# Kernel tuning notes

Hardware: AMD Instinct MI355X
Metric: run time of the kernel (lower is better)

Reference implementation:

```python
import jax, jax.numpy as jnp
import numpy as np


def setup_inputs() -> dict:
    key = jax.random.key(0)
    k1, k2, k3 = jax.random.split(key, 3)
    B, C, H, W = 4, 32, 320, 320
    NC = 21  # num_category
    return {
        "input_F": jax.random.normal(k1, (B, C, H, W), dtype=jnp.float32),
        "input_logit": jax.random.normal(k2, (B, NC, H, W), dtype=jnp.float32),
        "weight": jnp.asarray(1.0, dtype=jnp.float32),
        "compatibility": jax.random.normal(k3, (NC, NC, 1, 1), dtype=jnp.float32) * 0.1,
        "bias": jnp.zeros((NC,), dtype=jnp.float32),
        "kernel_len": 7,
    }


def _local_crf_pass(input_F, Q, weight, kernel_len):
    # Fused local_diff + exp-kernel + local_crf aggregation.
    # For each of the k*k neighborhood offsets (zero padding):
    #   diff[b,h,w]  = sum_c (F[b,c,h,w] - F_shift[b,c,h,w])^2 / C
    #   kern[b,h,w]  = weight * exp(-diff)
    #   out[b,q,h,w] += kern * Q_shift[b,q,h,w]
    B, C, H, W = input_F.shape
    pad = kernel_len // 2
    Fp = jnp.pad(input_F, ((0, 0), (0, 0), (pad, pad), (pad, pad)))
    Qp = jnp.pad(Q, ((0, 0), (0, 0), (pad, pad), (pad, pad)))
    out = jnp.zeros_like(Q)
    inv_c = jnp.float32(1.0 / C)
    for di in range(kernel_len):
        for dj in range(kernel_len):
            Fs = Fp[:, :, di:di + H, dj:dj + W]
            diff = jnp.sum((input_F - Fs) ** 2, axis=1) * inv_c  # [B,H,W]
            kern = weight * jnp.exp(-diff)
            out = out + kern[:, None, :, :] * Qp[:, :, di:di + H, dj:dj + W]
    return out / jnp.float32(kernel_len)


def reference(input_F, input_logit, weight, compatibility, bias, kernel_len):
    Q = jax.nn.softmax(input_logit, axis=1)  # softmax over categories
    out = _local_crf_pass(input_F, Q, weight, kernel_len)  # [B,NC,H,W]
    # 1x1 conv with sigmoid(compatibility) + bias
    compat = jax.nn.sigmoid(compatibility[:, :, 0, 0])  # [NC_out, NC_in]
    out = jnp.einsum('oi,bihw->bohw', compat, out) + bias[None, :, None, None]
    return input_logit - out
```

## Files before the change

### kernel.cpp

```cpp
#include <hip/hip_runtime.h>

#define Bn 4
#define Cn 32
#define Hn 320
#define Wn 320
#define NCn 21
#define PADn 3
#define TH 16
#define TW 64
#define HH 22
#define HWID 70
#define FW 71
#define QSTR 76
#define C2n 16
#define HWSZ (Hn*Wn)

typedef _Float16 h2 __attribute__((ext_vector_type(2)));

#define F_WORDS (C2n*HH*FW)
#define LDS_Q_OFF (F_WORDS*4)
#define LDS_TOTAL (LDS_Q_OFF + NCn*HH*QSTR)

__global__ __launch_bounds__(256, 1) void crf_fused(
    const float* __restrict__ Fin, const float* __restrict__ logit,
    const float* __restrict__ weight, const float* __restrict__ compat,
    const float* __restrict__ bias, float* __restrict__ out)
{
  extern __shared__ char smem[];
  uint32_t* fbuf = (uint32_t*)smem;
  uint8_t*  qbuf = (uint8_t*)(smem + LDS_Q_OFF);

  const int bid = blockIdx.x;
  const int b   = bid / 100;
  const int r   = bid % 100;
  const int th  = r / 5, twi = r % 5;
  const int h0  = th * TH, w0 = twi * TW;
  const int tid = threadIdx.x;

  const float* fb0 = Fin + (size_t)b * Cn * HWSZ;
  for (int idx = tid; idx < C2n * HH * HWID; idx += 256) {
    int lw = idx % HWID;
    int t2 = idx / HWID;
    int lh = t2 % HH;
    int c2 = t2 / HH;
    int gh = h0 - PADn + lh, gw = w0 - PADn + lw;
    uint32_t wd = 0u;
    if ((unsigned)gh < (unsigned)Hn && (unsigned)gw < (unsigned)Wn) {
      const float* p = fb0 + (size_t)(2 * c2) * HWSZ + gh * Wn + gw;
      float a0 = p[0], a1 = p[HWSZ];
      h2 hp; hp[0] = (_Float16)a0; hp[1] = (_Float16)a1;
      wd = __builtin_bit_cast(uint32_t, hp);
    }
    fbuf[(c2 * HH + lh) * FW + lw] = wd;
  }

  const float* lg0 = logit + (size_t)b * NCn * HWSZ;
  for (int p = tid; p < HH * HWID; p += 256) {
    int lw = p % HWID, lh = p / HWID;
    int gh = h0 - PADn + lh, gw = w0 - PADn + lw;
    uint8_t* qp = qbuf + lh * QSTR + lw;
    if ((unsigned)gh < (unsigned)Hn && (unsigned)gw < (unsigned)Wn) {
      const float* lp = lg0 + gh * Wn + gw;
      float v[NCn];
      float m = -1e30f;
      #pragma unroll
      for (int o = 0; o < NCn; o++) { v[o] = lp[(size_t)o * HWSZ]; m = fmaxf(m, v[o]); }
      float s = 0.f;
      #pragma unroll
      for (int o = 0; o < NCn; o++) { v[o] = __expf(v[o] - m); s += v[o]; }
      float inv = 1.0f / s;
      #pragma unroll
      for (int o = 0; o < NCn; o++) {
        int pk = __builtin_amdgcn_cvt_pk_fp8_f32(v[o] * inv, 0.f, 0, false);
        qp[o * HH * QSTR] = (uint8_t)(pk & 0xff);
      }
    } else {
      #pragma unroll
      for (int o = 0; o < NCn; o++) qp[o * HH * QSTR] = 0;
    }
  }
  __syncthreads();

  const int ty = tid >> 4;
  const int tg = tid & 15;
  const int x  = tg << 2;

  float acc[4][NCn];
  #pragma unroll
  for (int p = 0; p < 4; p++)
    #pragma unroll
    for (int o = 0; o < NCn; o++) acc[p][o] = 0.f;

  #pragma unroll 1
  for (int di = 0; di < 7; di++) {
    const int lhn = ty + di;
    float dsum[4][7];
    #pragma unroll
    for (int p = 0; p < 4; p++)
      #pragma unroll
      for (int j = 0; j < 7; j++) dsum[p][j] = 0.f;

    #pragma unroll 2
    for (int c2 = 0; c2 < C2n; c2++) {
      const uint32_t* frow = fbuf + (c2 * HH + lhn) * FW + x;
      const uint32_t* fcen = fbuf + (c2 * HH + (ty + PADn)) * FW + x + PADn;
      uint32_t nw[10], cw[4];
      #pragma unroll
      for (int j = 0; j < 10; j++) nw[j] = frow[j];
      #pragma unroll
      for (int p = 0; p < 4; p++) cw[p] = fcen[p];
      #pragma unroll
      for (int p = 0; p < 4; p++) {
        h2 c = __builtin_bit_cast(h2, cw[p]);
        #pragma unroll
        for (int j = 0; j < 7; j++) {
          h2 n = __builtin_bit_cast(h2, nw[p + j]);
          h2 d = c - n;
#if __has_builtin(__builtin_amdgcn_fdot2)
          dsum[p][j] = __builtin_amdgcn_fdot2(d, d, dsum[p][j], false);
#else
          float d0 = (float)d[0], d1 = (float)d[1];
          dsum[p][j] += d0 * d0 + d1 * d1;
#endif
        }
      }
    }
    #pragma unroll
    for (int p = 0; p < 4; p++)
      #pragma unroll
      for (int j = 0; j < 7; j++)
        dsum[p][j] = __expf(dsum[p][j] * -0.03125f);

    #pragma unroll
    for (int o = 0; o < NCn; o++) {
      const uint32_t* qrow = (const uint32_t*)(qbuf + (o * HH + lhn) * QSTR + x);
      uint32_t q0 = qrow[0], q1 = qrow[1], q2 = qrow[2];
      float qv[10];
      qv[0] = __builtin_amdgcn_cvt_f32_fp8((int)q0, 0);
      qv[1] = __builtin_amdgcn_cvt_f32_fp8((int)q0, 1);
      qv[2] = __builtin_amdgcn_cvt_f32_fp8((int)q0, 2);
      qv[3] = __builtin_amdgcn_cvt_f32_fp8((int)q0, 3);
      qv[4] = __builtin_amdgcn_cvt_f32_fp8((int)q1, 0);
      qv[5] = __builtin_amdgcn_cvt_f32_fp8((int)q1, 1);
      qv[6] = __builtin_amdgcn_cvt_f32_fp8((int)q1, 2);
      qv[7] = __builtin_amdgcn_cvt_f32_fp8((int)q1, 3);
      qv[8] = __builtin_amdgcn_cvt_f32_fp8((int)q2, 0);
      qv[9] = __builtin_amdgcn_cvt_f32_fp8((int)q2, 1);
      #pragma unroll
      for (int p = 0; p < 4; p++)
        #pragma unroll
        for (int j = 0; j < 7; j++)
          acc[p][o] = fmaf(dsum[p][j], qv[p + j], acc[p][o]);
    }
  }

  __syncthreads();
  float* cmat = (float*)(smem + LDS_Q_OFF);
  {
    float wgt = weight[0] * (1.0f / 7.0f);
    for (int i = tid; i < NCn * NCn; i += 256) {
      float c = compat[i];
      cmat[i] = wgt / (1.f + __expf(-c));
    }
  }
  __syncthreads();

  const int gh = h0 + ty;
  const size_t pixoff = (size_t)b * NCn * HWSZ + (size_t)gh * Wn + (w0 + x);
  const float* lc = logit + pixoff;
  float* oc = out + pixoff;
  #pragma unroll
  for (int o = 0; o < NCn; o++) {
    float s0 = 0.f, s1 = 0.f, s2 = 0.f, s3 = 0.f;
    #pragma unroll
    for (int i2 = 0; i2 < NCn; i2++) {
      float cm = cmat[o * NCn + i2];
      s0 = fmaf(cm, acc[0][i2], s0);
      s1 = fmaf(cm, acc[1][i2], s1);
      s2 = fmaf(cm, acc[2][i2], s2);
      s3 = fmaf(cm, acc[3][i2], s3);
    }
    float bo = bias[o];
    const float4 lg = *(const float4*)(lc + (size_t)o * HWSZ);
    float4 rr;
    rr.x = lg.x - s0 - bo;
    rr.y = lg.y - s1 - bo;
    rr.z = lg.z - s2 - bo;
    rr.w = lg.w - s3 - bo;
    *(float4*)(oc + (size_t)o * HWSZ) = rr;
  }
}

extern "C" void kernel_launch(void* const* d_in, const int* in_sizes, int n_in,
                              void* d_out, int out_size, void* d_ws, size_t ws_size,
                              hipStream_t stream) {
  (void)in_sizes; (void)n_in; (void)out_size; (void)d_ws; (void)ws_size;
  const float* F      = (const float*)d_in[0];
  const float* logit  = (const float*)d_in[1];
  const float* weight = (const float*)d_in[2];
  const float* compat = (const float*)d_in[3];
  const float* bias   = (const float*)d_in[4];
  float* out = (float*)d_out;

  hipFuncSetAttribute((const void*)crf_fused,
                      hipFuncAttributeMaxDynamicSharedMemorySize, LDS_TOTAL);
  crf_fused<<<dim3(Bn * 100), dim3(256), LDS_TOTAL, stream>>>(
      F, logit, weight, compat, bias, out);
}
```

Before: 283.8 us.

## Store features as FP8 in LDS, enlarge tile to 32x64, cache center features

After: 250.7 us. 11.7% less time.

```diff
diff --git a/kernel.cpp b/kernel.cpp
--- a/kernel.cpp
+++ b/kernel.cpp
@@ -5,60 +5,80 @@
 #define Hn 320
 #define Wn 320
 #define NCn 21
-#define PADn 3
-#define TH 16
-#define TW 64
-#define HH 22
-#define HWID 70
-#define FW 71
-#define QSTR 76
-#define C2n 16
 #define HWSZ (Hn*Wn)
 
+#define THr 32
+#define TWr 64
+#define HHr 38
+#define HWIDr 70
+#define FWr 72
+#define NG 8
+#define QSTRr 76
+
 typedef _Float16 h2 __attribute__((ext_vector_type(2)));
 
-#define F_WORDS (C2n*HH*FW)
-#define LDS_Q_OFF (F_WORDS*4)
-#define LDS_TOTAL (LDS_Q_OFF + NCn*HH*QSTR)
-
-__global__ __launch_bounds__(256, 1) void crf_fused(
+#define LDS_F   (NG*HHr*FWr*4)
+#define LDS_Q   (NCn*HHr*QSTRr)
+#define LDS_TOTAL (LDS_F + LDS_Q)
+
+__device__ __forceinline__ h2 fp8pair_lo(uint32_t w) {
+  uint32_t t = ((w & 0x000000FFu) << 8) | ((w & 0x0000FF00u) << 16);
+  uint32_t r = (t & 0x80008000u) | ((t >> 1) & 0x3FFF3FFFu);
+  return __builtin_bit_cast(h2, r);
+}
+__device__ __forceinline__ h2 fp8pair_hi(uint32_t w) {
+  uint32_t t = ((w >> 8) & 0x0000FF00u) | (w & 0xFF000000u);
+  uint32_t r = (t & 0x80008000u) | ((t >> 1) & 0x3FFF3FFFu);
+  return __builtin_bit_cast(h2, r);
+}
+
+__device__ __forceinline__ float fdot2f(h2 a, h2 b, float c) {
+#if __has_builtin(__builtin_amdgcn_fdot2)
+  return __builtin_amdgcn_fdot2(a, b, c, false);
+#else
+  return c + (float)a[0]*(float)b[0] + (float)a[1]*(float)b[1];
+#endif
+}
+
+__global__ __launch_bounds__(512, 1) void crf_fused2(
     const float* __restrict__ Fin, const float* __restrict__ logit,
     const float* __restrict__ weight, const float* __restrict__ compat,
     const float* __restrict__ bias, float* __restrict__ out)
 {
   extern __shared__ char smem[];
   uint32_t* fbuf = (uint32_t*)smem;
-  uint8_t*  qbuf = (uint8_t*)(smem + LDS_Q_OFF);
+  uint8_t*  qbuf = (uint8_t*)(smem + LDS_F);
 
   const int bid = blockIdx.x;
-  const int b   = bid / 100;
-  const int r   = bid % 100;
+  const int b   = bid / 50;
+  const int r   = bid % 50;
   const int th  = r / 5, twi = r % 5;
-  const int h0  = th * TH, w0 = twi * TW;
+  const int h0  = th * THr, w0 = twi * TWr;
   const int tid = threadIdx.x;
 
   const float* fb0 = Fin + (size_t)b * Cn * HWSZ;
-  for (int idx = tid; idx < C2n * HH * HWID; idx += 256) {
-    int lw = idx % HWID;
-    int t2 = idx / HWID;
-    int lh = t2 % HH;
-    int c2 = t2 / HH;
-    int gh = h0 - PADn + lh, gw = w0 - PADn + lw;
+  for (int idx = tid; idx < NG * HHr * FWr; idx += 512) {
+    int lw = idx % FWr;
+    int r2 = idx / FWr;
+    int lh = r2 % HHr;
+    int g  = r2 / HHr;
+    int gh = h0 - 3 + lh, gw = w0 - 3 + lw;
     uint32_t wd = 0u;
-    if ((unsigned)gh < (unsigned)Hn && (unsigned)gw < (unsigned)Wn) {
-      const float* p = fb0 + (size_t)(2 * c2) * HWSZ + gh * Wn + gw;
-      float a0 = p[0], a1 = p[HWSZ];
-      h2 hp; hp[0] = (_Float16)a0; hp[1] = (_Float16)a1;
-      wd = __builtin_bit_cast(uint32_t, hp);
-    }
-    fbuf[(c2 * HH + lh) * FW + lw] = wd;
+    if (lw < HWIDr && (unsigned)gh < (unsigned)Hn && (unsigned)gw < (unsigned)Wn) {
+      const float* p = fb0 + (size_t)(4 * g) * HWSZ + gh * Wn + gw;
+      float f0 = p[0], f1 = p[HWSZ], f2 = p[2 * HWSZ], f3 = p[3 * HWSZ];
+      int pk = __builtin_amdgcn_cvt_pk_fp8_f32(f0, f1, 0, false);
+      pk = __builtin_amdgcn_cvt_pk_fp8_f32(f2, f3, pk, true);
+      wd = (uint32_t)pk;
+    }
+    fbuf[idx] = wd;
   }
 
   const float* lg0 = logit + (size_t)b * NCn * HWSZ;
-  for (int p = tid; p < HH * HWID; p += 256) {
-    int lw = p % HWID, lh = p / HWID;
-    int gh = h0 - PADn + lh, gw = w0 - PADn + lw;
-    uint8_t* qp = qbuf + lh * QSTR + lw;
+  for (int p = tid; p < HHr * HWIDr; p += 512) {
+    int lw = p % HWIDr, lh = p / HWIDr;
+    int gh = h0 - 3 + lh, gw = w0 - 3 + lw;
+    uint8_t* qp = qbuf + lh * QSTRr + lw;
     if ((unsigned)gh < (unsigned)Hn && (unsigned)gw < (unsigned)Wn) {
       const float* lp = lg0 + gh * Wn + gw;
       float v[NCn];
@@ -72,11 +92,11 @@
       #pragma unroll
       for (int o = 0; o < NCn; o++) {
         int pk = __builtin_amdgcn_cvt_pk_fp8_f32(v[o] * inv, 0.f, 0, false);
-        qp[o * HH * QSTR] = (uint8_t)(pk & 0xff);
+        qp[(size_t)o * HHr * QSTRr] = (uint8_t)(pk & 0xff);
       }
     } else {
       #pragma unroll
-      for (int o = 0; o < NCn; o++) qp[o * HH * QSTR] = 0;
+      for (int o = 0; o < NCn; o++) qp[(size_t)o * HHr * QSTRr] = 0;
     }
   }
   __syncthreads();
@@ -85,6 +105,18 @@
   const int tg = tid & 15;
   const int x  = tg << 2;
 
+  h2 cen[NG][8];
+  #pragma unroll
+  for (int g = 0; g < NG; g++) {
+    const uint32_t* fc = fbuf + (g * HHr + (ty + 3)) * FWr + (x + 3);
+    #pragma unroll
+    for (int p = 0; p < 4; p++) {
+      uint32_t w = fc[p];
+      cen[g][2 * p]     = fp8pair_lo(w);
+      cen[g][2 * p + 1] = fp8pair_hi(w);
+    }
+  }
+
   float acc[4][NCn];
   #pragma unroll
   for (int p = 0; p < 4; p++)
@@ -94,46 +126,46 @@
   #pragma unroll 1
   for (int di = 0; di < 7; di++) {
     const int lhn = ty + di;
-    float dsum[4][7];
+    float ds[4][7];
     #pragma unroll
     for (int p = 0; p < 4; p++)
       #pragma unroll
-      for (int j = 0; j < 7; j++) dsum[p][j] = 0.f;
-
-    #pragma unroll 2
-    for (int c2 = 0; c2 < C2n; c2++) {
-      const uint32_t* frow = fbuf + (c2 * HH + lhn) * FW + x;
-      const uint32_t* fcen = fbuf + (c2 * HH + (ty + PADn)) * FW + x + PADn;
-      uint32_t nw[10], cw[4];
-      #pragma unroll
-      for (int j = 0; j < 10; j++) nw[j] = frow[j];
-      #pragma unroll
-      for (int p = 0; p < 4; p++) cw[p] = fcen[p];
-      #pragma unroll
-      for (int p = 0; p < 4; p++) {
-        h2 c = __builtin_bit_cast(h2, cw[p]);
+      for (int j = 0; j < 7; j++) ds[p][j] = 0.f;
+
+    #pragma unroll
+    for (int g = 0; g < NG; g++) {
+      const uint32_t* frow = fbuf + (g * HHr + lhn) * FWr + x;
+      uint4 n0 = *(const uint4*)(frow);
+      uint4 n1 = *(const uint4*)(frow + 4);
+      uint4 n2 = *(const uint4*)(frow + 8);
+      uint32_t nw[10] = {n0.x, n0.y, n0.z, n0.w, n1.x, n1.y, n1.z, n1.w, n2.x, n2.y};
+      #pragma unroll
+      for (int k = 0; k < 10; k++) {
+        h2 lo = fp8pair_lo(nw[k]);
+        h2 hi = fp8pair_hi(nw[k]);
         #pragma unroll
-        for (int j = 0; j < 7; j++) {
-          h2 n = __builtin_bit_cast(h2, nw[p + j]);
-          h2 d = c - n;
-#if __has_builtin(__builtin_amdgcn_fdot2)
-          dsum[p][j] = __builtin_amdgcn_fdot2(d, d, dsum[p][j], false);
-#else
-          float d0 = (float)d[0], d1 = (float)d[1];
-          dsum[p][j] += d0 * d0 + d1 * d1;
-#endif
+        for (int p = 0; p < 4; p++) {
+          const int j = k - p;
+          if (j >= 0 && j < 7) {
+            h2 d0 = cen[g][2 * p] - lo;
+            h2 d1 = cen[g][2 * p + 1] - hi;
+            float t = fdot2f(d0, d0, ds[p][j]);
+            ds[p][j] = fdot2f(d1, d1, t);
+          }
         }
       }
     }
+
+    float kern[4][7];
     #pragma unroll
     for (int p = 0; p < 4; p++)
       #pragma unroll
       for (int j = 0; j < 7; j++)
-        dsum[p][j] = __expf(dsum[p][j] * -0.03125f);
+        kern[p][j] = __expf(ds[p][j] * -2048.0f);
 
     #pragma unroll
     for (int o = 0; o < NCn; o++) {
-      const uint32_t* qrow = (const uint32_t*)(qbuf + (o * HH + lhn) * QSTR + x);
+      const uint32_t* qrow = (const uint32_t*)(qbuf + (o * HHr + lhn) * QSTRr + x);
       uint32_t q0 = qrow[0], q1 = qrow[1], q2 = qrow[2];
       float qv[10];
       qv[0] = __builtin_amdgcn_cvt_f32_fp8((int)q0, 0);
@@ -150,15 +182,15 @@
       for (int p = 0; p < 4; p++)
         #pragma unroll
         for (int j = 0; j < 7; j++)
-          acc[p][o] = fmaf(dsum[p][j], qv[p + j], acc[p][o]);
+          acc[p][o] = fmaf(kern[p][j], qv[p + j], acc[p][o]);
     }
   }
 
   __syncthreads();
-  float* cmat = (float*)(smem + LDS_Q_OFF);
+  float* cmat = (float*)(smem + LDS_F);
   {
     float wgt = weight[0] * (1.0f / 7.0f);
-    for (int i = tid; i < NCn * NCn; i += 256) {
+    for (int i = tid; i < NCn * NCn; i += 512) {
       float c = compat[i];
       cmat[i] = wgt / (1.f + __expf(-c));
     }
@@ -202,8 +234,8 @@
   const float* bias   = (const float*)d_in[4];
   float* out = (float*)d_out;
 
-  hipFuncSetAttribute((const void*)crf_fused,
+  hipFuncSetAttribute((const void*)crf_fused2,
                       hipFuncAttributeMaxDynamicSharedMemorySize, LDS_TOTAL);
-  crf_fused<<<dim3(Bn * 100), dim3(256), LDS_TOTAL, stream>>>(
+  crf_fused2<<<dim3(Bn * 50), dim3(512), LDS_TOTAL, stream>>>(
       F, logit, weight, compat, bias, out);
 }
```
